# Kernel tuning notes

Hardware: AMD Instinct MI355X
Metric: run time of the kernel (lower is better)

The kernel has to match this reference:

```python
import jax, jax.numpy as jnp
import numpy as np

EPS = 1e-5
SLOPE = 0.01  # LeakyReLU default
C = 512
C2 = C // 2
B, D, W, H = 2, 16, 16, 16


def _leaky(x):
    return jnp.where(x >= 0, x, SLOPE * x)


def _bn_c(x, g, b, rm, rv):
    # per-channel BN (eval mode) over axis 1 of a (B,C,...) tensor
    shape = (1, -1) + (1,) * (x.ndim - 2)
    inv = jax.lax.rsqrt(rv + EPS)
    return (x - rm.reshape(shape)) * (inv * g).reshape(shape) + b.reshape(shape)


def _bn_s(x, g, b, rm, rv):
    # scalar-feature BatchNorm1d(1) in eval mode
    return (x - rm[0]) * (jax.lax.rsqrt(rv[0] + EPS) * g[0]) + b[0]


def setup_inputs() -> dict:
    key = jax.random.key(0)
    ks = jax.random.split(key, 8)
    s = 0.02
    inp = {
        'x': jax.random.normal(ks[0], (B, C, D, W, H), jnp.float32),
        'topo_prompt': jax.random.normal(ks[1], (D, W, H, 6), jnp.float32) * s,
        # edge_aggregation_func: Linear(6,1)+BN1d(1)
        'w_ea': jax.random.normal(ks[2], (1, 6), jnp.float32) * s,
        'b_ea': jnp.zeros((1,), jnp.float32),
        'g_ea': jnp.ones((1,), jnp.float32), 'be_ea': jnp.zeros((1,), jnp.float32),
        'rm_ea': jnp.zeros((1,), jnp.float32), 'rv_ea': jnp.ones((1,), jnp.float32),
        # vertex_update_func: Linear(2C, C/2)+BN1d(C/2)
        'w_v': jax.random.normal(ks[3], (C2, 2 * C), jnp.float32) * s,
        'b_v': jnp.zeros((C2,), jnp.float32),
        'g_v': jnp.ones((C2,), jnp.float32), 'be_v': jnp.zeros((C2,), jnp.float32),
        'rm_v': jnp.zeros((C2,), jnp.float32), 'rv_v': jnp.ones((C2,), jnp.float32),
        # edge_update_func: Linear(2C, C/2)+BN1d(C/2)
        'w_e': jax.random.normal(ks[4], (C2, 2 * C), jnp.float32) * s,
        'b_e': jnp.zeros((C2,), jnp.float32),
        'g_e': jnp.ones((C2,), jnp.float32), 'be_e': jnp.zeros((C2,), jnp.float32),
        'rm_e': jnp.zeros((C2,), jnp.float32), 'rv_e': jnp.ones((C2,), jnp.float32),
        # update_edge_reduce_func: Linear(6,1)+BN1d(1)
        'w_r': jax.random.normal(ks[5], (1, 6), jnp.float32) * s,
        'b_r': jnp.zeros((1,), jnp.float32),
        'g_r': jnp.ones((1,), jnp.float32), 'be_r': jnp.zeros((1,), jnp.float32),
        'rm_r': jnp.zeros((1,), jnp.float32), 'rv_r': jnp.ones((1,), jnp.float32),
        # final_aggregation_layer: Conv3d(3C/2 -> C, k=1, bias=False)+BN3d(C)
        'w_f': jax.random.normal(ks[6], (C, C + C2), jnp.float32) * s,
        'g_f': jnp.ones((C,), jnp.float32), 'be_f': jnp.zeros((C,), jnp.float32),
        'rm_f': jnp.zeros((C,), jnp.float32), 'rv_f': jnp.ones((C,), jnp.float32),
    }
    return inp


def reference(x, topo_prompt,
              w_ea, b_ea, g_ea, be_ea, rm_ea, rv_ea,
              w_v, b_v, g_v, be_v, rm_v, rv_v,
              w_e, b_e, g_e, be_e, rm_e, rv_e,
              w_r, b_r, g_r, be_r, rm_r, rv_r,
              w_f, g_f, be_f, rm_f, rv_f):
    # 6-neighbor circular shifts: cat((x[-1:], x[:-1])) == roll(+1); cat((x[1:], x[:1])) == roll(-1)
    shifts = jnp.stack([
        jnp.roll(x, 1, axis=2), jnp.roll(x, -1, axis=2),
        jnp.roll(x, 1, axis=3), jnp.roll(x, -1, axis=3),
        jnp.roll(x, 1, axis=4), jnp.roll(x, -1, axis=4),
    ], axis=-1)  # (B,C,D,W,H,6)
    edge = shifts * x[..., None] + topo_prompt  # topo_prompt (D,W,H,6) broadcasts

    # edge aggregation: Linear(6->1) + BN1d(1) + LeakyReLU
    agg = jnp.einsum('bcdwhk,k->bcdwh', edge, w_ea[0]) + b_ea[0]
    agg = _leaky(_bn_s(agg, g_ea, be_ea, rm_ea, rv_ea))  # (B,C,D,W,H)

    # vertex update: Linear(2C->C/2) + BN + LeakyReLU
    feat_v = jnp.concatenate([x, agg], axis=1)  # (B,2C,D,W,H)
    uv = jnp.einsum('bcdwh,oc->bodwh', feat_v, w_v) + b_v[None, :, None, None, None]
    uv = _leaky(_bn_c(uv, g_v, be_v, rm_v, rv_v))  # (B,C/2,D,W,H)

    # edge update: cat(vertex x6, edge) on channel dim -> Linear(2C->C/2) + BN + LeakyReLU
    vrep = jnp.broadcast_to(x[..., None], x.shape + (6,))
    feat_e = jnp.concatenate([vrep, edge], axis=1)  # (B,2C,D,W,H,6)
    ue = jnp.einsum('bcdwhk,oc->bodwhk', feat_e, w_e) + b_e[None, :, None, None, None, None]
    ue = _leaky(_bn_c(ue, g_e, be_e, rm_e, rv_e))  # (B,C/2,D,W,H,6)

    # reduce 6 neighbors: Linear(6->1) + BN1d(1) + LeakyReLU
    ur = jnp.einsum('bodwhk,k->bodwh', ue, w_r[0]) + b_r[0]
    ur = _leaky(_bn_s(ur, g_r, be_r, rm_r, rv_r))  # (B,C/2,D,W,H)

    update_feature = uv * ur

    # final 1x1x1 conv (bias=False) + BN3d + LeakyReLU
    fused = jnp.concatenate([x, update_feature], axis=1)  # (B,3C/2,D,W,H)
    out = jnp.einsum('bcdwh,oc->bodwh', fused, w_f)
    out = _leaky(_bn_c(out, g_f, be_f, rm_f, rv_f))
    return out
```

## Files before the change

kernel.cpp:

```cpp
#include <hip/hip_runtime.h>

#define BATCH 2
#define C 512
#define C2 256
#define V 4096
#define NROWS 8192
#define EPS 1e-5f
#define SLOPE 0.01f

typedef __bf16 bf16;
typedef __bf16 bf16x8 __attribute__((ext_vector_type(8)));
typedef __bf16 bf16x4 __attribute__((ext_vector_type(4)));
typedef float  f32x4  __attribute__((ext_vector_type(4)));

__device__ __forceinline__ float leaky(float x) { return x >= 0.f ? x : SLOPE * x; }

__device__ __forceinline__ int nbr(int v, int k) {
    int h = v & 15, w = (v >> 4) & 15, d = v >> 8;
    switch (k) {
        case 0: return (v & 0x0FF) | (((d + 15) & 15) << 8);
        case 1: return (v & 0x0FF) | (((d + 1) & 15) << 8);
        case 2: return (v & 0xF0F) | (((w + 15) & 15) << 4);
        case 3: return (v & 0xF0F) | (((w + 1) & 15) << 4);
        case 4: return (v & 0xFF0) | ((h + 15) & 15);
        default: return (v & 0xFF0) | ((h + 1) & 15);
    }
}

__device__ __forceinline__ void gload16(const bf16* g, bf16* l) {
    __builtin_amdgcn_global_load_lds(
        (const __attribute__((address_space(1))) void*)g,
        (__attribute__((address_space(3))) void*)l, 16, 0, 0);
}

__device__ __forceinline__ void stage_gl64(bf16* buf, const bf16* srcbase, size_t ld,
                                           int kcol, int wv, int lane) {
    const int sslot = ((lane & 7) ^ (lane >> 3)) * 8;
    #pragma unroll
    for (int j = 0; j < 4; j++) {
        const int rl = wv * 32 + j * 8;
        gload16(srcbase + (size_t)(rl + (lane >> 3)) * ld + kcol + sslot,
                buf + rl * 64);
    }
}

__device__ __forceinline__ void mmstep64(const bf16* A, const bf16* B,
                                         f32x4 (&acc)[4][4], int abase, int bbase,
                                         int lr, int kg)
{
    #pragma unroll
    for (int sub = 0; sub < 2; sub++) {
        const int slot = ((sub * 4 + kg) ^ (lr & 7)) * 8;
        bf16x8 af[4], bv[4];
        #pragma unroll
        for (int mb = 0; mb < 4; mb++)
            af[mb] = *(const bf16x8*)(A + (abase + mb * 16 + lr) * 64 + slot);
        #pragma unroll
        for (int nb = 0; nb < 4; nb++)
            bv[nb] = *(const bf16x8*)(B + (bbase + nb * 16 + lr) * 64 + slot);
        #pragma unroll
        for (int mb = 0; mb < 4; mb++)
            #pragma unroll
            for (int nb = 0; nb < 4; nb++)
                acc[mb][nb] = __builtin_amdgcn_mfma_f32_16x16x32_bf16(af[mb], bv[nb], acc[mb][nb], 0, 0, 0);
    }
}

__global__ __launch_bounds__(256) void k_prep(
    const float* wv, const float* we, const float* wf,
    const float* w_ea, const float* b_ea, const float* g_ea, const float* be_ea,
    const float* rm_ea, const float* rv_ea,
    const float* b_v, const float* g_v, const float* be_v, const float* rm_v, const float* rv_v,
    const float* b_e, const float* g_e, const float* be_e, const float* rm_e, const float* rv_e,
    const float* w_r, const float* b_r, const float* g_r, const float* be_r,
    const float* rm_r, const float* rv_r,
    const float* g_f, const float* be_f, const float* rm_f, const float* rv_f,
    float* P, float* obv, float* obe, float* obf,
    bf16* wmain, bf16* we2, bf16* owf)
{
    int i = blockIdx.x * 256 + threadIdx.x;
    if (i < 524288) {
        int o = i >> 10, c = i & 1023;
        float val;
        if (o < 256) val = rsqrtf(rv_v[o] + EPS) * g_v[o] * wv[(size_t)o * 1024 + c];
        else {
            int oe = o - 256;
            val = (c < 512) ? rsqrtf(rv_e[oe] + EPS) * g_e[oe] * we[(size_t)oe * 1024 + c] : 0.f;
        }
        wmain[i] = (bf16)val;
    } else if (i < 655360) {
        int j = i - 524288; int o = j >> 9, c = j & 511;
        we2[j] = (bf16)(rsqrtf(rv_e[o] + EPS) * g_e[o] * we[(size_t)o * 1024 + 512 + c]);
    } else if (i < 1048576) {
        int j = i - 655360; int o = j / 768;
        owf[j] = (bf16)(rsqrtf(rv_f[o] + EPS) * g_f[o] * wf[j]);
    }
    if (blockIdx.x == 0) {
        int t = threadIdx.x;
        obf[t]       = be_f[t]       - rsqrtf(rv_f[t]       + EPS) * g_f[t]       * rm_f[t];
        obf[t + 256] = be_f[t + 256] - rsqrtf(rv_f[t + 256] + EPS) * g_f[t + 256] * rm_f[t + 256];
        float sv = rsqrtf(rv_v[t] + EPS) * g_v[t];
        obv[t] = sv * (b_v[t] - rm_v[t]) + be_v[t];
        float se = rsqrtf(rv_e[t] + EPS) * g_e[t];
        obe[t] = se * (b_e[t] - rm_e[t]) + be_e[t];
        if (t < 6) {
            float sa = rsqrtf(rv_ea[0] + EPS) * g_ea[0];
            P[t] = sa * w_ea[t];
            float sr = rsqrtf(rv_r[0] + EPS) * g_r[0];
            P[8 + t] = sr * w_r[t];
        }
        if (t == 6) {
            float sa = rsqrtf(rv_ea[0] + EPS) * g_ea[0];
            P[6] = sa * (b_ea[0] - rm_ea[0]) + be_ea[0];
            float sr = rsqrtf(rv_r[0] + EPS) * g_r[0];
            P[14] = sr * (b_r[0] - rm_r[0]) + be_r[0];
        }
    }
}

__global__ __launch_bounds__(256) void k_aggT(
    const float* __restrict__ x, const float* __restrict__ topo,
    const float* __restrict__ P,
    bf16* __restrict__ xT, bf16* __restrict__ aggT)
{
    __shared__ float T[64][65];
    const int t = threadIdx.x;
    const int b = blockIdx.z, ct = blockIdx.y * 64, vt = blockIdx.x * 64;
    const int cl = t >> 2;
    const int c  = ct + cl;
    const int vl0 = (t & 3) * 16;
    const int v0 = vt + vl0;
    const int w = (v0 >> 4) & 15, d = v0 >> 8;
    const float* xp = x + (((size_t)b * C + c) << 12);

    float xr[16], xd0[16], xd1[16], xw0[16], xw1[16];
    #pragma unroll
    for (int i = 0; i < 4; i++) {
        float4 a;
        a = ((const float4*)(xp + v0))[i];                        xr [4*i]=a.x; xr [4*i+1]=a.y; xr [4*i+2]=a.z; xr [4*i+3]=a.w;
        a = ((const float4*)(xp + (((d+15)&15)<<8) + (w<<4)))[i]; xd0[4*i]=a.x; xd0[4*i+1]=a.y; xd0[4*i+2]=a.z; xd0[4*i+3]=a.w;
        a = ((const float4*)(xp + (((d+ 1)&15)<<8) + (w<<4)))[i]; xd1[4*i]=a.x; xd1[4*i+1]=a.y; xd1[4*i+2]=a.z; xd1[4*i+3]=a.w;
        a = ((const float4*)(xp + (d<<8) + (((w+15)&15)<<4)))[i]; xw0[4*i]=a.x; xw0[4*i+1]=a.y; xw0[4*i+2]=a.z; xw0[4*i+3]=a.w;
        a = ((const float4*)(xp + (d<<8) + (((w+ 1)&15)<<4)))[i]; xw1[4*i]=a.x; xw1[4*i+1]=a.y; xw1[4*i+2]=a.z; xw1[4*i+3]=a.w;
    }

    #pragma unroll
    for (int p = 0; p < 2; ++p) {
        float val[16];
        if (p == 0) {
            #pragma unroll
            for (int j = 0; j < 16; j++) val[j] = xr[j];
        } else {
            #pragma unroll
            for (int j = 0; j < 16; j++) {
                const float* tp = topo + (size_t)(v0 + j) * 6;
                float s = P[6];
                s = fmaf(P[0], fmaf(xd0[j], xr[j], tp[0]), s);
                s = fmaf(P[1], fmaf(xd1[j], xr[j], tp[1]), s);
                s = fmaf(P[2], fmaf(xw0[j], xr[j], tp[2]), s);
                s = fmaf(P[3], fmaf(xw1[j], xr[j], tp[3]), s);
                s = fmaf(P[4], fmaf(xr[(j+15)&15], xr[j], tp[4]), s);
                s = fmaf(P[5], fmaf(xr[(j+ 1)&15], xr[j], tp[5]), s);
                val[j] = leaky(s);
            }
        }
        __syncthreads();
        #pragma unroll
        for (int j = 0; j < 16; j++) T[cl][vl0 + j] = val[j];
        __syncthreads();
        const int vr = t >> 2, c0 = (t & 3) * 16;
        bf16x8 lo, hi;
        #pragma unroll
        for (int i = 0; i < 8; i++) {
            lo[i] = (bf16)T[c0 + i][vr];
            hi[i] = (bf16)T[c0 + 8 + i][vr];
        }
        bf16* dst = (p == 0) ? xT : aggT;
        bf16* dp = dst + ((size_t)(b << 12) + vt + vr) * C + ct + c0;
        *(bf16x8*)dp = lo;
        *(bf16x8*)(dp + 8) = hi;
    }
}

template<bool MAIN>
__device__ __forceinline__ void gemm_body(
    int m0, int n0, int kk, int nsteps,
    const bf16* __restrict__ wA, size_t ldA,
    const bf16* __restrict__ xT, const bf16* __restrict__ aggT,
    const float* __restrict__ topo, const float* __restrict__ bvp,
    bf16* __restrict__ uvT, float* __restrict__ sxe, bf16* __restrict__ se,
    bf16 (*A)[128 * 64], bf16 (*B)[128 * 64])
{
    const int t = threadIdx.x, lane = t & 63;
    const int wv = t >> 6, wmi = wv >> 1, wni = wv & 1;
    const int lr = lane & 15, kg = lane >> 4;

    const bf16* wAb  = wA + (size_t)m0 * ldA;
    const bf16* xTb  = xT + (size_t)n0 * C;
    const bf16* agTb = aggT + (size_t)n0 * C;

    const int erow = t >> 1, ecol = (t & 1) * 32;
    const bf16* pBx = nullptr; const bf16* pB2 = nullptr; float tp = 0.f;
    int eslot[4];
    if (!MAIN) {
        const int rB = n0 + erow;
        const int vvv = rB & 4095, bb = rB >> 12;
        pBx = xT + (size_t)rB * C + ecol;
        pB2 = xT + (size_t)((bb << 12) | nbr(vvv, kk)) * C + ecol;
        tp = topo[vvv * 6 + kk];
        #pragma unroll
        for (int j = 0; j < 4; j++)
            eslot[j] = ((((t & 1) * 4 + j) ^ (erow & 7)) * 8);
    }

    f32x4 acc[4][4];
    #pragma unroll
    for (int mb = 0; mb < 4; mb++)
        #pragma unroll
        for (int nb = 0; nb < 4; nb++) acc[mb][nb] = 0.f;

    uint4 bx[4], bn[4];
    auto issueB = [&](int s) {
        #pragma unroll
        for (int j = 0; j < 4; j++) {
            bx[j] = *(const uint4*)(pBx + s * 64 + j * 8);
            bn[j] = *(const uint4*)(pB2 + s * 64 + j * 8);
        }
    };
    auto commitB = [&](int buf) {
        #pragma unroll
        for (int j = 0; j < 4; j++) {
            bf16x8 xa = *(bf16x8*)&bx[j], xn = *(bf16x8*)&bn[j];
            bf16x8 e;
            #pragma unroll
            for (int i = 0; i < 8; i++)
                e[i] = (bf16)fmaf((float)xa[i], (float)xn[i], tp);
            *(bf16x8*)(&B[buf][erow * 64 + eslot[j]]) = e;
        }
    };
    auto stageStep = [&](int buf, int s) {
        stage_gl64(A[buf], wAb, ldA, s * 64, wv, lane);
        if (MAIN) {
            const bf16* src = (s < 8) ? xTb : agTb;
            stage_gl64(B[buf], src, C, (s & 7) * 64, wv, lane);
        }
    };

    stageStep(0, 0);
    if (!MAIN) { issueB(0); commitB(0); if (nsteps > 1) issueB(1); }

    int cb = 0;
    #pragma unroll 1
    for (int s = 0; s < nsteps; ++s) {
        __syncthreads();
        if (s + 1 < nsteps) stageStep(cb ^ 1, s + 1);
        mmstep64(A[cb], B[cb], acc, wmi * 64, wni * 64, lr, kg);
        if (!MAIN && s + 1 < nsteps) {
            commitB(cb ^ 1);
            if (s + 2 < nsteps) issueB(s + 2);
        }
        cb ^= 1;
    }

    if (MAIN) {
        if (m0 < 256) {
            #pragma unroll
            for (int mb = 0; mb < 4; mb++) {
                const int o = m0 + wmi * 64 + mb * 16 + kg * 4;
                f32x4 bv4 = *(const f32x4*)(bvp + o);
                #pragma unroll
                for (int nb = 0; nb < 4; nb++) {
                    const int col = n0 + wni * 64 + nb * 16 + lr;
                    bf16x4 o4;
                    #pragma unroll
                    for (int q = 0; q < 4; q++)
                        o4[q] = (bf16)leaky(acc[mb][nb][q] + bv4[q]);
                    *(bf16x4*)(uvT + (size_t)col * C2 + o) = o4;
                }
            }
        } else {
            #pragma unroll
            for (int mb = 0; mb < 4; mb++) {
                const int o = (m0 - 256) + wmi * 64 + mb * 16 + kg * 4;
                #pragma unroll
                for (int nb = 0; nb < 4; nb++) {
                    const int col = n0 + wni * 64 + nb * 16 + lr;
                    *(f32x4*)(sxe + (size_t)col * C2 + o) = acc[mb][nb];
                }
            }
        }
    } else {
        #pragma unroll
        for (int mb = 0; mb < 4; mb++) {
            const int o = m0 + wmi * 64 + mb * 16 + kg * 4;
            #pragma unroll
            for (int nb = 0; nb < 4; nb++) {
                const int col = n0 + wni * 64 + nb * 16 + lr;
                bf16x4 o4;
                #pragma unroll
                for (int q = 0; q < 4; q++) o4[q] = (bf16)acc[mb][nb][q];
                *(bf16x4*)(se + ((size_t)kk * NROWS + col) * C2 + o) = o4;
            }
        }
    }
}

__global__ __launch_bounds__(256, 2) void k_gemm(
    const bf16* __restrict__ xT, const bf16* __restrict__ aggT,
    const bf16* __restrict__ wm, const bf16* __restrict__ we2,
    const float* __restrict__ bvp, const float* __restrict__ topo,
    bf16* __restrict__ uvT, float* __restrict__ sxe, bf16* __restrict__ se)
{
    __shared__ __align__(16) bf16 A[2][128 * 64];
    __shared__ __align__(16) bf16 B[2][128 * 64];
    const int lb = (blockIdx.x & 7) * 128 + (blockIdx.x >> 3);
    const int n0 = (lb >> 4) * 128;
    const int sub = lb & 15;
    if (sub < 4) {
        const int m0 = sub * 128;
        const int nsteps = (m0 < 256) ? 16 : 8;
        gemm_body<true>(m0, n0, 0, nsteps, wm, 1024, xT, aggT, topo, bvp,
                        uvT, sxe, nullptr, A, B);
    } else {
        const int e = sub - 4;
        const int kk = e >> 1, m0 = (e & 1) * 128;
        gemm_body<false>(m0, n0, kk, 8, we2, 512, xT, aggT, topo, bvp,
                         nullptr, nullptr, se, A, B);
    }
}

__global__ __launch_bounds__(256) void k_comb(
    const float* __restrict__ sxe, const bf16* __restrict__ se,
    const bf16* __restrict__ uvT, const float* __restrict__ bep,
    const float* __restrict__ P, bf16* __restrict__ updT)
{
    const int g = blockIdx.x * 256 + threadIdx.x;
    const int row = g >> 5, o0 = (g & 31) * 8;
    const size_t base = (size_t)row * C2 + o0;

    f32x4 sx0 = *(const f32x4*)(sxe + base);
    f32x4 sx1 = *(const f32x4*)(sxe + base + 4);
    f32x4 be0 = *(const f32x4*)(bep + o0);
    f32x4 be1 = *(const f32x4*)(bep + o0 + 4);
    float ur[8] = {};
    #pragma unroll
    for (int k = 0; k < 6; k++) {
        bf16x8 s8 = *(const bf16x8*)(se + (size_t)k * NROWS * C2 + base);
        const float wrk = P[8 + k];
        #pragma unroll
        for (int i = 0; i < 4; i++) {
            ur[i]     = fmaf(wrk, leaky(sx0[i] + (float)s8[i]     + be0[i]), ur[i]);
            ur[i + 4] = fmaf(wrk, leaky(sx1[i] + (float)s8[i + 4] + be1[i]), ur[i + 4]);
        }
    }
    const float brp = P[14];
    bf16x8 uv8 = *(const bf16x8*)(uvT + base);
    bf16x8 o8;
    #pragma unroll
    for (int i = 0; i < 8; i++)
        o8[i] = (bf16)((float)uv8[i] * leaky(ur[i] + brp));
    *(bf16x8*)(updT + base) = o8;
}

__global__ __launch_bounds__(256, 2) void k_out(
    const bf16* __restrict__ xT, const bf16* __restrict__ updT,
    const bf16* __restrict__ wf, const float* __restrict__ bfp,
    float* __restrict__ out)
{
    __shared__ __align__(16) bf16 A[2][128 * 64];
    __shared__ __align__(16) bf16 B[2][128 * 64];
    const int t = threadIdx.x, lane = t & 63;
    const int wv = t >> 6, wmi = wv >> 1, wni = wv & 1;
    const int lr = lane & 15, kg = lane >> 4;
    const int lb = (blockIdx.x & 7) * 32 + (blockIdx.x >> 3);
    const int n0 = (lb >> 2) * 128, m0 = (lb & 3) * 128;

    const bf16* wAb = wf   + (size_t)m0 * 768;
    const bf16* xTb = xT   + (size_t)n0 * C;
    const bf16* uTb = updT + (size_t)n0 * C2;

    f32x4 acc[4][4];
    #pragma unroll
    for (int mb = 0; mb < 4; mb++)
        #pragma unroll
        for (int nb = 0; nb < 4; nb++) acc[mb][nb] = 0.f;

    auto stageStep = [&](int buf, int s) {
        stage_gl64(A[buf], wAb, 768, s * 64, wv, lane);
        if (s < 8) stage_gl64(B[buf], xTb, C, s * 64, wv, lane);
        else       stage_gl64(B[buf], uTb, C2, (s - 8) * 64, wv, lane);
    };

    stageStep(0, 0);
    int cb = 0;
    #pragma unroll 1
    for (int s = 0; s < 12; ++s) {
        __syncthreads();
        if (s + 1 < 12) stageStep(cb ^ 1, s + 1);
        mmstep64(A[cb], B[cb], acc, wmi * 64, wni * 64, lr, kg);
        cb ^= 1;
    }

    #pragma unroll
    for (int mb = 0; mb < 4; mb++) {
        const int o = m0 + wmi * 64 + mb * 16 + kg * 4;
        f32x4 bf4 = *(const f32x4*)(bfp + o);
        #pragma unroll
        for (int nb = 0; nb < 4; nb++) {
            const int col = n0 + wni * 64 + nb * 16 + lr;
            const int b = col >> 12, v = col & 4095;
            #pragma unroll
            for (int q = 0; q < 4; q++)
                out[(((size_t)b * C + o + q) << 12) + v] = leaky(acc[mb][nb][q] + bf4[q]);
        }
    }
}

extern "C" void kernel_launch(void* const* d_in, const int* in_sizes, int n_in,
                              void* d_out, int out_size, void* d_ws, size_t ws_size,
                              hipStream_t stream)
{
    const float* x    = (const float*)d_in[0];
    const float* topo = (const float*)d_in[1];
    const float* w_ea = (const float*)d_in[2];
    const float* b_ea = (const float*)d_in[3];
    const float* g_ea = (const float*)d_in[4];
    const float* be_ea= (const float*)d_in[5];
    const float* rm_ea= (const float*)d_in[6];
    const float* rv_ea= (const float*)d_in[7];
    const float* w_v  = (const float*)d_in[8];
    const float* b_v  = (const float*)d_in[9];
    const float* g_v  = (const float*)d_in[10];
    const float* be_v = (const float*)d_in[11];
    const float* rm_v = (const float*)d_in[12];
    const float* rv_v = (const float*)d_in[13];
    const float* w_e  = (const float*)d_in[14];
    const float* b_e  = (const float*)d_in[15];
    const float* g_e  = (const float*)d_in[16];
    const float* be_e = (const float*)d_in[17];
    const float* rm_e = (const float*)d_in[18];
    const float* rv_e = (const float*)d_in[19];
    const float* w_r  = (const float*)d_in[20];
    const float* b_r  = (const float*)d_in[21];
    const float* g_r  = (const float*)d_in[22];
    const float* be_r = (const float*)d_in[23];
    const float* rm_r = (const float*)d_in[24];
    const float* rv_r = (const float*)d_in[25];
    const float* w_f  = (const float*)d_in[26];
    const float* g_f  = (const float*)d_in[27];
    const float* be_f = (const float*)d_in[28];
    const float* rm_f = (const float*)d_in[29];
    const float* rv_f = (const float*)d_in[30];

    char* base = (char*)d_ws;
    size_t off = 0;
    auto take = [&](size_t bytes) { size_t r = off; off = (off + bytes + 255) & ~(size_t)255; return r; };
    float* P    = (float*)(base + take(64 * 4));
    float* bvp  = (float*)(base + take(256 * 4));
    float* bep  = (float*)(base + take(256 * 4));
    float* bfp  = (float*)(base + take(512 * 4));
    bf16*  wmp  = (bf16*)(base + take((size_t)524288 * 2));
    bf16*  we2p = (bf16*)(base + take((size_t)131072 * 2));
    bf16*  wfp  = (bf16*)(base + take((size_t)393216 * 2));
    bf16*  xT   = (bf16*)(base + take((size_t)NROWS * C * 2));
    bf16*  aggT = (bf16*)(base + take((size_t)NROWS * C * 2));
    bf16*  uvT  = (bf16*)(base + take((size_t)NROWS * C2 * 2));
    bf16*  updT = (bf16*)(base + take((size_t)NROWS * C2 * 2));
    float* sxe  = (float*)(base + take((size_t)NROWS * C2 * 4));
    bf16*  se   = (bf16*)(base + take((size_t)6 * NROWS * C2 * 2));

    k_prep<<<4096, 256, 0, stream>>>(
        w_v, w_e, w_f,
        w_ea, b_ea, g_ea, be_ea, rm_ea, rv_ea,
        b_v, g_v, be_v, rm_v, rv_v,
        b_e, g_e, be_e, rm_e, rv_e,
        w_r, b_r, g_r, be_r, rm_r, rv_r,
        g_f, be_f, rm_f, rv_f,
        P, bvp, bep, bfp, wmp, we2p, wfp);

    k_aggT<<<dim3(64, 8, 2), 256, 0, stream>>>(x, topo, P, xT, aggT);

    k_gemm<<<dim3(1024), 256, 0, stream>>>(xT, aggT, wmp, we2p, bvp, topo, uvT, sxe, se);
    k_comb<<<dim3(NROWS * C2 / 8 / 256), 256, 0, stream>>>(sxe, se, uvT, bep, P, updT);
    k_out<<<dim3(256), 256, 0, stream>>>(xT, updT, wfp, bfp, (float*)d_out);
}
```

Baseline: 96.05 us.

## Use K=32 tiles with triple-buffered LDS pipeline and explicit waitcnt barriers

The fused GEMM kernel now stages K slices of 32 instead of 64 and triple-buffers A and B in LDS. The single per-step __syncthreads is replaced by explicit s_waitcnt vmcnt plus s_barrier, so global loads run two steps ahead of the MFMA work. Shared memory per block shrinks from 64 KiB to 48 KiB, and the launch-bounds occupancy hint rises from 2 to 3 blocks per CU. In exchange there are twice as many barrier steps with less MFMA work per step, and the hand-counted vmcnt values must match exactly how many loads each path issues.

```diff
diff --git a/kernel.cpp b/kernel.cpp
--- a/kernel.cpp
+++ b/kernel.cpp
@@ -33,6 +33,35 @@
         (__attribute__((address_space(3))) void*)l, 16, 0, 0);
 }
 
+__device__ __forceinline__ void stage32(bf16* buf, const bf16* src, size_t ld,
+                                        int kcol, int wv, int lane) {
+    const int sslot = ((lane & 3) ^ ((lane >> 2) & 3)) * 8;
+    #pragma unroll
+    for (int j = 0; j < 2; j++) {
+        const int rl = wv * 32 + j * 16;
+        gload16(src + (size_t)(rl + (lane >> 2)) * ld + kcol + sslot, buf + rl * 32);
+    }
+}
+
+__device__ __forceinline__ void mm32(const bf16* A, const bf16* B,
+                                     f32x4 (&acc)[4][4], int abase, int bbase,
+                                     int lr, int kg)
+{
+    const int aslot = (kg ^ (lr & 3)) * 8;
+    bf16x8 af[4], bv[4];
+    #pragma unroll
+    for (int mb = 0; mb < 4; mb++)
+        af[mb] = *(const bf16x8*)(A + (abase + mb * 16 + lr) * 32 + aslot);
+    #pragma unroll
+    for (int nb = 0; nb < 4; nb++)
+        bv[nb] = *(const bf16x8*)(B + (bbase + nb * 16 + lr) * 32 + aslot);
+    #pragma unroll
+    for (int mb = 0; mb < 4; mb++)
+        #pragma unroll
+        for (int nb = 0; nb < 4; nb++)
+            acc[mb][nb] = __builtin_amdgcn_mfma_f32_16x16x32_bf16(af[mb], bv[nb], acc[mb][nb], 0, 0, 0);
+}
+
 __device__ __forceinline__ void stage_gl64(bf16* buf, const bf16* srcbase, size_t ld,
                                            int kcol, int wv, int lane) {
     const int sslot = ((lane & 7) ^ (lane >> 3)) * 8;
@@ -43,7 +72,6 @@
                 buf + rl * 64);
     }
 }
-
 __device__ __forceinline__ void mmstep64(const bf16* A, const bf16* B,
                                          f32x4 (&acc)[4][4], int abase, int bbase,
                                          int lr, int kg)
@@ -189,7 +217,7 @@
     const bf16* __restrict__ xT, const bf16* __restrict__ aggT,
     const float* __restrict__ topo, const float* __restrict__ bvp,
     bf16* __restrict__ uvT, float* __restrict__ sxe, bf16* __restrict__ se,
-    bf16 (*A)[128 * 64], bf16 (*B)[128 * 64])
+    bf16 (*A)[128 * 32], bf16 (*B)[128 * 32])
 {
     const int t = threadIdx.x, lane = t & 63;
     const int wv = t >> 6, wmi = wv >> 1, wni = wv & 1;
@@ -199,18 +227,17 @@
     const bf16* xTb  = xT + (size_t)n0 * C;
     const bf16* agTb = aggT + (size_t)n0 * C;
 
-    const int erow = t >> 1, ecol = (t & 1) * 32;
+    const int er = t >> 1, ech = t & 1;
     const bf16* pBx = nullptr; const bf16* pB2 = nullptr; float tp = 0.f;
-    int eslot[4];
+    int es0 = 0, es1 = 0;
     if (!MAIN) {
-        const int rB = n0 + erow;
+        const int rB = n0 + er;
         const int vvv = rB & 4095, bb = rB >> 12;
-        pBx = xT + (size_t)rB * C + ecol;
-        pB2 = xT + (size_t)((bb << 12) | nbr(vvv, kk)) * C + ecol;
+        pBx = xT + (size_t)rB * C + ech * 16;
+        pB2 = xT + (size_t)((bb << 12) | nbr(vvv, kk)) * C + ech * 16;
         tp = topo[vvv * 6 + kk];
-        #pragma unroll
-        for (int j = 0; j < 4; j++)
-            eslot[j] = ((((t & 1) * 4 + j) ^ (erow & 7)) * 8);
+        es0 = (((ech * 2 + 0) ^ (er & 3)) * 8);
+        es1 = (((ech * 2 + 1) ^ (er & 3)) * 8);
     }
 
     f32x4 acc[4][4];
@@ -219,47 +246,56 @@
         #pragma unroll
         for (int nb = 0; nb < 4; nb++) acc[mb][nb] = 0.f;
 
-    uint4 bx[4], bn[4];
-    auto issueB = [&](int s) {
-        #pragma unroll
-        for (int j = 0; j < 4; j++) {
-            bx[j] = *(const uint4*)(pBx + s * 64 + j * 8);
-            bn[j] = *(const uint4*)(pB2 + s * 64 + j * 8);
-        }
+    uint4 bx0, bx1, bn0, bn1;
+    auto issueE = [&](int s) {
+        bx0 = *(const uint4*)(pBx + s * 32);
+        bx1 = *(const uint4*)(pBx + s * 32 + 8);
+        bn0 = *(const uint4*)(pB2 + s * 32);
+        bn1 = *(const uint4*)(pB2 + s * 32 + 8);
     };
-    auto commitB = [&](int buf) {
-        #pragma unroll
-        for (int j = 0; j < 4; j++) {
-            bf16x8 xa = *(bf16x8*)&bx[j], xn = *(bf16x8*)&bn[j];
-            bf16x8 e;
-            #pragma unroll
-            for (int i = 0; i < 8; i++)
-                e[i] = (bf16)fmaf((float)xa[i], (float)xn[i], tp);
-            *(bf16x8*)(&B[buf][erow * 64 + eslot[j]]) = e;
-        }
+    auto commitE = [&](bf16* Bb) {
+        bf16x8 xa = *(bf16x8*)&bx0, xn = *(bf16x8*)&bn0, e;
+        #pragma unroll
+        for (int i = 0; i < 8; i++) e[i] = (bf16)fmaf((float)xa[i], (float)xn[i], tp);
+        *(bf16x8*)(&Bb[er * 32 + es0]) = e;
+        xa = *(bf16x8*)&bx1; xn = *(bf16x8*)&bn1;
+        #pragma unroll
+        for (int i = 0; i < 8; i++) e[i] = (bf16)fmaf((float)xa[i], (float)xn[i], tp);
+        *(bf16x8*)(&Bb[er * 32 + es1]) = e;
     };
-    auto stageStep = [&](int buf, int s) {
-        stage_gl64(A[buf], wAb, ldA, s * 64, wv, lane);
-        if (MAIN) {
-            const bf16* src = (s < 8) ? xTb : agTb;
-            stage_gl64(B[buf], src, C, (s & 7) * 64, wv, lane);
-        }
+    auto stageMain = [&](int buf, int s) {
+        stage32(A[buf], wAb, ldA, s * 32, wv, lane);
+        const bf16* src = (s < 16) ? xTb : agTb;
+        stage32(B[buf], src, C, (s & 15) * 32, wv, lane);
     };
 
-    stageStep(0, 0);
-    if (!MAIN) { issueB(0); commitB(0); if (nsteps > 1) issueB(1); }
-
-    int cb = 0;
-    #pragma unroll 1
-    for (int s = 0; s < nsteps; ++s) {
-        __syncthreads();
-        if (s + 1 < nsteps) stageStep(cb ^ 1, s + 1);
-        mmstep64(A[cb], B[cb], acc, wmi * 64, wni * 64, lr, kg);
-        if (!MAIN && s + 1 < nsteps) {
-            commitB(cb ^ 1);
-            if (s + 2 < nsteps) issueB(s + 2);
-        }
-        cb ^= 1;
+    if (MAIN) {
+        stageMain(0, 0);
+        if (nsteps > 1) stageMain(1, 1);
+        #pragma unroll 1
+        for (int s = 0; s < nsteps; ++s) {
+            if (s + 1 < nsteps) asm volatile("s_waitcnt vmcnt(4)" ::: "memory");
+            else                asm volatile("s_waitcnt vmcnt(0)" ::: "memory");
+            __builtin_amdgcn_s_barrier();
+            if (s + 2 < nsteps) stageMain((s + 2) % 3, s + 2);
+            mm32(A[s % 3], B[s % 3], acc, wmi * 64, wni * 64, lr, kg);
+        }
+    } else {
+        stage32(A[0], wAb, ldA, 0, wv, lane);
+        issueE(0);
+        if (nsteps > 1) stage32(A[1], wAb, ldA, 32, wv, lane);
+        #pragma unroll 1
+        for (int s = 0; s < nsteps; ++s) {
+            if (s + 1 < nsteps) asm volatile("s_waitcnt vmcnt(2)" ::: "memory");
+            else                asm volatile("s_waitcnt vmcnt(0)" ::: "memory");
+            commitE(B[s & 1]);
+            asm volatile("s_waitcnt lgkmcnt(0)" ::: "memory");
+            __builtin_amdgcn_s_barrier();
+            if (s + 1 < nsteps) issueE(s + 1);
+            if (s + 2 < nsteps) stage32(A[(s + 2) % 3], wAb, ldA, (s + 2) * 32, wv, lane);
+            mm32(A[s % 3], B[s & 1], acc, wmi * 64, wni * 64, lr, kg);
+            __builtin_amdgcn_s_barrier();
+        }
     }
 
     if (MAIN) {
@@ -305,26 +341,26 @@
     }
 }
 
-__global__ __launch_bounds__(256, 2) void k_gemm(
+__global__ __launch_bounds__(256, 3) void k_gemm(
     const bf16* __restrict__ xT, const bf16* __restrict__ aggT,
     const bf16* __restrict__ wm, const bf16* __restrict__ we2,
     const float* __restrict__ bvp, const float* __restrict__ topo,
     bf16* __restrict__ uvT, float* __restrict__ sxe, bf16* __restrict__ se)
 {
-    __shared__ __align__(16) bf16 A[2][128 * 64];
-    __shared__ __align__(16) bf16 B[2][128 * 64];
+    __shared__ __align__(16) bf16 A[3][128 * 32];
+    __shared__ __align__(16) bf16 B[3][128 * 32];
     const int lb = (blockIdx.x & 7) * 128 + (blockIdx.x >> 3);
     const int n0 = (lb >> 4) * 128;
     const int sub = lb & 15;
     if (sub < 4) {
         const int m0 = sub * 128;
-        const int nsteps = (m0 < 256) ? 16 : 8;
+        const int nsteps = (m0 < 256) ? 32 : 16;
         gemm_body<true>(m0, n0, 0, nsteps, wm, 1024, xT, aggT, topo, bvp,
                         uvT, sxe, nullptr, A, B);
     } else {
         const int e = sub - 4;
         const int kk = e >> 1, m0 = (e & 1) * 128;
-        gemm_body<false>(m0, n0, kk, 8, we2, 512, xT, aggT, topo, bvp,
+        gemm_body<false>(m0, n0, kk, 16, we2, 512, xT, aggT, topo, bvp,
                          nullptr, nullptr, se, A, B);
     }
 }
```

After: 103.1 us. 1.07x slower.
